# Performance work log

Hardware: AMD Instinct MI355X
Metric: run time of the kernel (lower is better)

Reference implementation:

```python
import jax, jax.numpy as jnp
import numpy as np

# Static config matching init_kwargs
WZ, WH, WW = 2, 6, 12          # window size
MZ, MH, MW = 4, 16, 15          # ceil(input_shape / window_size) for (8,96,180)
HEADS, DIM, B = 6, 192, 1
DH = DIM // HEADS
P = WZ * WH * WW                # 144 tokens per window
WN = MZ * MH * MW               # 960 windows
WT = MZ * MH                    # 64 window types
SCALE = DH ** -0.5
TABLE = WZ * WZ * WH * WH * (2 * WW - 1)  # 3312 bias entries


def _position_index():
    zi = np.arange(WZ); zj = -np.arange(WZ) * WZ
    hi = np.arange(WH); hj = -np.arange(WH) * WH
    w = np.arange(WW)
    c1 = np.stack(np.meshgrid(zi, hi, w, indexing='ij')).reshape(3, -1)  # (3, P)
    c2 = np.stack(np.meshgrid(zj, hj, w, indexing='ij')).reshape(3, -1)  # (3, P)
    coords = (c1[:, :, None] - c2[:, None, :]).transpose(1, 2, 0)        # (P, P, 3)
    coords[:, :, 2] += WW - 1
    coords[:, :, 1] *= 2 * WW - 1
    coords[:, :, 0] *= (2 * WW - 1) * WH * WH
    return coords.sum(-1).reshape(-1)  # (P*P,)

POS_IDX = jnp.asarray(_position_index())


def setup_inputs() -> dict:
    key = jax.random.key(0)
    ks = jax.random.split(key, 5)
    x = jax.random.normal(ks[0], (B * WN, P, DIM), dtype=jnp.float32)
    mask = jnp.zeros((WN, P, P), dtype=jnp.float32)
    w_qkv = jax.random.normal(ks[1], (DIM, 3 * DIM), dtype=jnp.float32) * 0.02
    w_proj = jax.random.normal(ks[2], (DIM, DIM), dtype=jnp.float32) * 0.02
    b_proj = jnp.zeros((DIM,), dtype=jnp.float32)
    bias_table = jax.random.normal(ks[3], (TABLE, WT, HEADS), dtype=jnp.float32) * 0.02
    return {"x": x, "mask": mask, "w_qkv": w_qkv, "w_proj": w_proj,
            "b_proj": b_proj, "bias_table": bias_table}


def reference(x, mask, w_qkv, w_proj, b_proj, bias_table):
    BN = x.shape[0]  # B*WN
    qkv = (x @ w_qkv).reshape(BN, P, 3, HEADS, DH).transpose(2, 0, 3, 1, 4)  # (3,BN,h,P,dh)
    q, k, v = SCALE * qkv[0], qkv[1], qkv[2]
    attn = jnp.einsum('bhid,bhjd->bhij', q, k)  # (BN, h, P, P)
    # (B mZ mH mW) h P P -> (B mW) (mZ mH) h P P
    attn = attn.reshape(B, MZ, MH, MW, HEADS, P, P)
    attn = attn.transpose(0, 3, 1, 2, 4, 5, 6).reshape(B * MW, WT, HEADS, P, P)
    # gather earth-specific bias: (P*P, WT, h) -> (WT, h, P, P)
    bias = bias_table[POS_IDX].reshape(P, P, WT, HEADS).transpose(2, 3, 0, 1)
    attn = attn + bias  # broadcast over (B mW)
    # back to (B mZ mH mW) h P P
    attn = attn.reshape(B, MW, MZ, MH, HEADS, P, P)
    attn = attn.transpose(0, 2, 3, 1, 4, 5, 6).reshape(B, WN, HEADS, P, P)
    attn = attn + mask[None, :, None]  # (1, wN, 1, P, P)
    attn = jax.nn.softmax(attn, axis=-1).reshape(B * WN, HEADS, P, P)
    out = jnp.einsum('bhij,bhjd->bhid', attn, v)           # (BN, h, P, dh)
    out = out.transpose(0, 2, 1, 3).reshape(BN, P, DIM)    # merge heads
    return out @ w_proj + b_proj
```

## Files before the change

### kernel.cpp

```cpp
#include <hip/hip_runtime.h>

#define HEADS 6
#define DIM 192
#define DH 32
#define PW 144
#define WN 960
#define MWD 15
#define NTOK (WN*PW)
#define SCALE 0.17677669529663687f

typedef __attribute__((ext_vector_type(8))) short bf16x8;
typedef __attribute__((ext_vector_type(4))) short bf16x4;
typedef __attribute__((ext_vector_type(4))) float f32x4;

#define MFMA16(a,b,c) __builtin_amdgcn_mfma_f32_16x16x32_bf16(a,b,c,0,0,0)

__device__ __forceinline__ unsigned short f2bf(float f) {
    unsigned int u = __builtin_bit_cast(unsigned int, f);
    u += 0x7fffu + ((u >> 16) & 1u);
    return (unsigned short)(u >> 16);
}
__device__ __forceinline__ float bf2f(unsigned short s) {
    unsigned int u = ((unsigned int)s) << 16;
    return __builtin_bit_cast(float, u);
}

__global__ void prep_weights(const float* __restrict__ wqkv,
                             const float* __restrict__ wproj,
                             unsigned short* __restrict__ wqkvT,
                             unsigned short* __restrict__ wprojT) {
    int t = blockIdx.x * 256 + threadIdx.x;
    if (t < 576 * 192) {
        int n = t / 192, k = t % 192;
        wqkvT[t] = f2bf(wqkv[k * 576 + n]);
    } else {
        int t2 = t - 576 * 192;
        int n = t2 / 192, k = t2 % 192;
        wprojT[t2] = f2bf(wproj[k * 192 + n]);
    }
}

__global__ void prep_bias(const float* __restrict__ table,
                          unsigned short* __restrict__ bias_d) {
    int t = blockIdx.x * 256 + threadIdx.x;
    int j = t % 144;
    int i = (t / 144) % 144;
    int h = (t / 20736) % 6;
    int wt = t / 124416;
    int z1 = i / 72, h1 = (i / 12) % 6, w1 = i % 12;
    int z2 = j / 72, h2 = (j / 12) % 6, w2 = j % 12;
    int pos = (z1 + 2 * z2) * 828 + (h1 + 6 * h2) * 23 + (w1 - w2 + 11);
    bias_d[t] = f2bf(table[pos * 384 + wt * 6 + h]);
}

__global__ __launch_bounds__(256) void prep_cast(const float* __restrict__ x,
                                                 unsigned short* __restrict__ xb) {
    long long c = (long long)blockIdx.x * 256 + threadIdx.x;
    const float* p = x + c * 8;
    f32x4 v0 = *(const f32x4*)p;
    f32x4 v1 = *(const f32x4*)(p + 4);
    bf16x8 o;
    o[0] = (short)f2bf(v0[0]); o[1] = (short)f2bf(v0[1]);
    o[2] = (short)f2bf(v0[2]); o[3] = (short)f2bf(v0[3]);
    o[4] = (short)f2bf(v1[0]); o[5] = (short)f2bf(v1[1]);
    o[6] = (short)f2bf(v1[2]); o[7] = (short)f2bf(v1[3]);
    *(bf16x8*)(xb + c * 8) = o;
}

__global__ __launch_bounds__(256) void qkv_gemm(
        const unsigned short* __restrict__ xb, const unsigned short* __restrict__ wqkvT,
        unsigned short* __restrict__ qb, unsigned short* __restrict__ kb,
        unsigned short* __restrict__ vtb) {
    __shared__ unsigned short A[64 * 200];
    __shared__ unsigned short Bt[96 * 200];
    int bid = blockIdx.x;
    int r8 = bid & 7, s = bid >> 3;
    int nblk = s % 6;
    int mtile = r8 * 270 + s / 6;
    int tid = threadIdx.x;

    const unsigned short* xp = xb + (long long)mtile * (64 * 192);
    #pragma unroll
    for (int it = 0; it < 6; ++it) {
        int c = tid + it * 256;
        int row = c / 24, c8 = (c % 24) * 8;
        *(bf16x8*)&A[row * 200 + c8] = *(const bf16x8*)(xp + c * 8);
    }
    const unsigned short* wp = wqkvT + nblk * (96 * 192);
    #pragma unroll
    for (int it = 0; it < 9; ++it) {
        int c = tid + it * 256;
        int row = c / 24, c8 = (c % 24) * 8;
        *(bf16x8*)&Bt[row * 200 + c8] = *(const bf16x8*)(wp + c * 8);
    }
    __syncthreads();

    int lane = tid & 63, wv = tid >> 6;
    int l16 = lane & 15, quad = lane >> 4;
    f32x4 acc[6];
    #pragma unroll
    for (int i = 0; i < 6; ++i) acc[i] = (f32x4){0.f, 0.f, 0.f, 0.f};

    #pragma unroll
    for (int kc = 0; kc < 6; ++kc) {
        bf16x8 af = *(const bf16x8*)&A[(wv * 16 + l16) * 200 + kc * 32 + quad * 8];
        #pragma unroll
        for (int ct = 0; ct < 6; ++ct) {
            bf16x8 bfr = *(const bf16x8*)&Bt[(ct * 16 + l16) * 200 + kc * 32 + quad * 8];
            acc[ct] = MFMA16(af, bfr, acc[ct]);
        }
    }

    int token0 = mtile * 64 + wv * 16 + quad * 4;
    int win = token0 / 144;
    int p0 = token0 - win * 144;
    #pragma unroll
    for (int ct = 0; ct < 6; ++ct) {
        int c0 = nblk * 96 + ct * 16;
        int which = c0 / 192;
        int head = (c0 % 192) / 32;
        int d = (c0 % 32) + l16;
        if (which == 0) {
            int base = ((win * 6 + head) * 144 + p0) * 32 + d;
            #pragma unroll
            for (int r = 0; r < 4; ++r) qb[base + r * 32] = f2bf(acc[ct][r]);
        } else if (which == 1) {
            int base = ((win * 6 + head) * 144 + p0) * 32 + d;
            #pragma unroll
            for (int r = 0; r < 4; ++r) kb[base + r * 32] = f2bf(acc[ct][r]);
        } else {
            int base = ((win * 6 + head) * 32 + d) * 144 + p0;
            bf16x4 o;
            #pragma unroll
            for (int r = 0; r < 4; ++r) o[r] = (short)f2bf(acc[ct][r]);
            *(bf16x4*)&vtb[base] = o;
        }
    }
}

__global__ __launch_bounds__(192) void attn(
        const unsigned short* __restrict__ qb, const unsigned short* __restrict__ kb,
        const unsigned short* __restrict__ vtb, const unsigned short* __restrict__ bias_d,
        const float* __restrict__ mask, unsigned short* __restrict__ Ob) {
    __shared__ unsigned short Q[144 * 40];
    __shared__ unsigned short Kl[144 * 40];
    __shared__ unsigned short Vt[32 * 160];
    __shared__ unsigned short Pl[3 * 16 * 168];

    int bx = blockIdx.x;
    int r8 = bx & 7, s = bx >> 3;
    int h = s % 6;
    int win = r8 * 120 + s / 6;
    int wt = win / MWD;
    int tid = threadIdx.x;
    int lane = tid & 63, wv = tid >> 6;
    int l16 = lane & 15, quad = lane >> 4;

    int qoff = (win * 6 + h) * (144 * 32);
    #pragma unroll
    for (int it = 0; it < 3; ++it) {
        int c = tid + it * 192;
        int row = c >> 2, c8 = (c & 3) * 8;
        *(bf16x8*)&Q[row * 40 + c8]  = *(const bf16x8*)(qb + qoff + c * 8);
        *(bf16x8*)&Kl[row * 40 + c8] = *(const bf16x8*)(kb + qoff + c * 8);
        int vr = c / 18, vc = (c % 18) * 8;
        *(bf16x8*)&Vt[vr * 160 + vc] = *(const bf16x8*)(vtb + qoff + c * 8);
    }
    {
        int row = lane >> 2, ch = lane & 3;
        *(bf16x4*)&Pl[wv * 2688 + row * 168 + 144 + ch * 4] = (bf16x4){0, 0, 0, 0};
    }
    if (tid < 64) {
        int row = tid >> 1, off = 144 + (tid & 1) * 8;
        *(bf16x8*)&Vt[row * 160 + off] = (bf16x8){0, 0, 0, 0, 0, 0, 0, 0};
    }
    __syncthreads();

    const float* maskp = mask + win * 20736;
    const unsigned short* biasp = bias_d + (wt * 6 + h) * 20736;
    const f32x4 z = {0.f, 0.f, 0.f, 0.f};

    for (int rt = 0; rt < 3; ++rt) {
        int i0 = (wv * 3 + rt) * 16;
        bf16x8 aq = *(const bf16x8*)&Q[(i0 + l16) * 40 + quad * 8];
        f32x4 sreg[9];
        #pragma unroll
        for (int ct = 0; ct < 9; ++ct) {
            bf16x8 bk = *(const bf16x8*)&Kl[(ct * 16 + l16) * 40 + quad * 8];
            sreg[ct] = MFMA16(aq, bk, z);
        }
        #pragma unroll
        for (int ct = 0; ct < 9; ++ct) {
            int j = ct * 16 + l16;
            #pragma unroll
            for (int r = 0; r < 4; ++r) {
                int i = i0 + quad * 4 + r;
                float b = bf2f(biasp[i * 144 + j]);
                float mk = maskp[i * 144 + j];
                sreg[ct][r] = sreg[ct][r] * SCALE + b + mk;
            }
        }
        #pragma unroll
        for (int r = 0; r < 4; ++r) {
            float mx = sreg[0][r];
            #pragma unroll
            for (int ct = 1; ct < 9; ++ct) mx = fmaxf(mx, sreg[ct][r]);
            #pragma unroll
            for (int off = 1; off < 16; off <<= 1) mx = fmaxf(mx, __shfl_xor(mx, off, 64));
            float sum = 0.f;
            #pragma unroll
            for (int ct = 0; ct < 9; ++ct) { float e = __expf(sreg[ct][r] - mx); sreg[ct][r] = e; sum += e; }
            #pragma unroll
            for (int off = 1; off < 16; off <<= 1) sum += __shfl_xor(sum, off, 64);
            float inv = 1.0f / sum;
            #pragma unroll
            for (int ct = 0; ct < 9; ++ct) sreg[ct][r] *= inv;
        }
        int pb = wv * 2688;
        #pragma unroll
        for (int ct = 0; ct < 9; ++ct) {
            #pragma unroll
            for (int r = 0; r < 4; ++r)
                Pl[pb + (quad * 4 + r) * 168 + ct * 16 + l16] = f2bf(sreg[ct][r]);
        }
        f32x4 o0 = z, o1 = z;
        #pragma unroll
        for (int kc = 0; kc < 5; ++kc) {
            bf16x8 ap = *(const bf16x8*)&Pl[pb + l16 * 168 + kc * 32 + quad * 8];
            bf16x8 b0 = *(const bf16x8*)&Vt[l16 * 160 + kc * 32 + quad * 8];
            bf16x8 b1 = *(const bf16x8*)&Vt[(16 + l16) * 160 + kc * 32 + quad * 8];
            o0 = MFMA16(ap, b0, o0);
            o1 = MFMA16(ap, b1, o1);
        }
        #pragma unroll
        for (int r = 0; r < 4; ++r) {
            int i = i0 + quad * 4 + r;
            int ob = (win * 144 + i) * 192 + h * 32 + l16;
            Ob[ob] = f2bf(o0[r]);
            Ob[ob + 16] = f2bf(o1[r]);
        }
    }
}

__global__ __launch_bounds__(256) void out_gemm(
        const unsigned short* __restrict__ Ob, const unsigned short* __restrict__ wprojT,
        const float* __restrict__ bproj, float* __restrict__ out) {
    __shared__ unsigned short A[64 * 200];
    __shared__ unsigned short Bt[96 * 200];
    int bid = blockIdx.x;
    int r8 = bid & 7, s = bid >> 3;
    int nblk = s % 2;
    int mtile = r8 * 270 + s / 2;
    int tid = threadIdx.x;

    const unsigned short* op = Ob + (long long)mtile * (64 * 192);
    #pragma unroll
    for (int it = 0; it < 6; ++it) {
        int c = tid + it * 256;
        int row = c / 24, c8 = (c % 24) * 8;
        *(bf16x8*)&A[row * 200 + c8] = *(const bf16x8*)(op + c * 8);
    }
    const unsigned short* wp = wprojT + nblk * (96 * 192);
    #pragma unroll
    for (int it = 0; it < 9; ++it) {
        int c = tid + it * 256;
        int row = c / 24, c8 = (c % 24) * 8;
        *(bf16x8*)&Bt[row * 200 + c8] = *(const bf16x8*)(wp + c * 8);
    }
    __syncthreads();

    int lane = tid & 63, wv = tid >> 6;
    int l16 = lane & 15, quad = lane >> 4;
    f32x4 acc[6];
    #pragma unroll
    for (int i = 0; i < 6; ++i) acc[i] = (f32x4){0.f, 0.f, 0.f, 0.f};
    #pragma unroll
    for (int kc = 0; kc < 6; ++kc) {
        bf16x8 af = *(const bf16x8*)&A[(wv * 16 + l16) * 200 + kc * 32 + quad * 8];
        #pragma unroll
        for (int ct = 0; ct < 6; ++ct) {
            bf16x8 bfr = *(const bf16x8*)&Bt[(ct * 16 + l16) * 200 + kc * 32 + quad * 8];
            acc[ct] = MFMA16(af, bfr, acc[ct]);
        }
    }
    int token0 = mtile * 64 + wv * 16 + quad * 4;
    #pragma unroll
    for (int ct = 0; ct < 6; ++ct) {
        int c = nblk * 96 + ct * 16 + l16;
        float bp = bproj[c];
        #pragma unroll
        for (int r = 0; r < 4; ++r)
            out[(token0 + r) * 192 + c] = acc[ct][r] + bp;
    }
}

extern "C" void kernel_launch(void* const* d_in, const int* in_sizes, int n_in,
                              void* d_out, int out_size, void* d_ws, size_t ws_size,
                              hipStream_t stream) {
    const float* x     = (const float*)d_in[0];
    const float* mask  = (const float*)d_in[1];
    const float* wqkv  = (const float*)d_in[2];
    const float* wproj = (const float*)d_in[3];
    const float* bproj = (const float*)d_in[4];
    const float* btab  = (const float*)d_in[5];
    float* out = (float*)d_out;

    char* ws = (char*)d_ws;
    unsigned short* xb     = (unsigned short*)(ws + 0);
    unsigned short* Ob     = (unsigned short*)(ws + 0);
    unsigned short* qb     = (unsigned short*)(ws + 53084160);
    unsigned short* kb     = (unsigned short*)(ws + 106168320);
    unsigned short* vtb    = (unsigned short*)(ws + 159252480);
    unsigned short* bias_d = (unsigned short*)(ws + 212336640);
    unsigned short* wqkvT  = (unsigned short*)(ws + 228261888);
    unsigned short* wprojT = (unsigned short*)(ws + 228483072);

    prep_weights<<<576, 256, 0, stream>>>(wqkv, wproj, wqkvT, wprojT);
    prep_bias<<<31104, 256, 0, stream>>>(btab, bias_d);
    prep_cast<<<12960, 256, 0, stream>>>(x, xb);
    qkv_gemm<<<12960, 256, 0, stream>>>(xb, wqkvT, qb, kb, vtb);
    attn<<<5760, 192, 0, stream>>>(qb, kb, vtb, bias_d, mask, Ob);
    out_gemm<<<4320, 256, 0, stream>>>(Ob, wprojT, bproj, out);
}
```

Measured before the change: 486.0 us.

## Pre-permute bias and mask into MFMA fragment layout and fuse x cast into QKV GEMM

Bias and mask are rearranged by prep kernels into per-lane contiguous bf16 fragments matching the MFMA accumulator layout, so attn loads them with a few 16-byte vector loads instead of scattered scalar loads. The mask is converted to bf16, halving its traffic in attn, at the cost of an extra full pass over the fp32 mask each call and reduced mask precision. The separate fp32-to-bf16 cast kernel for x is folded into the QKV GEMM tile load, removing an intermediate buffer round trip. Q is read directly from global memory rather than staged in LDS, and attn gets an occupancy hint.

```diff
diff --git a/kernel.cpp b/kernel.cpp
--- a/kernel.cpp
+++ b/kernel.cpp
@@ -6,7 +6,6 @@
 #define PW 144
 #define WN 960
 #define MWD 15
-#define NTOK (WN*PW)
 #define SCALE 0.17677669529663687f
 
 typedef __attribute__((ext_vector_type(8))) short bf16x8;
@@ -40,35 +39,53 @@
     }
 }
 
-__global__ void prep_bias(const float* __restrict__ table,
-                          unsigned short* __restrict__ bias_d) {
+__global__ __launch_bounds__(256) void prep_biasR(const float* __restrict__ table,
+                                                  unsigned short* __restrict__ biasR) {
     int t = blockIdx.x * 256 + threadIdx.x;
-    int j = t % 144;
-    int i = (t / 144) % 144;
-    int h = (t / 20736) % 6;
-    int wt = t / 124416;
-    int z1 = i / 72, h1 = (i / 12) % 6, w1 = i % 12;
-    int z2 = j / 72, h2 = (j / 12) % 6, w2 = j % 12;
-    int pos = (z1 + 2 * z2) * 828 + (h1 + 6 * h2) * 23 + (w1 - w2 + 11);
-    bias_d[t] = f2bf(table[pos * 384 + wt * 6 + h]);
-}
-
-__global__ __launch_bounds__(256) void prep_cast(const float* __restrict__ x,
-                                                 unsigned short* __restrict__ xb) {
-    long long c = (long long)blockIdx.x * 256 + threadIdx.x;
-    const float* p = x + c * 8;
-    f32x4 v0 = *(const f32x4*)p;
-    f32x4 v1 = *(const f32x4*)(p + 4);
-    bf16x8 o;
-    o[0] = (short)f2bf(v0[0]); o[1] = (short)f2bf(v0[1]);
-    o[2] = (short)f2bf(v0[2]); o[3] = (short)f2bf(v0[3]);
-    o[4] = (short)f2bf(v1[0]); o[5] = (short)f2bf(v1[1]);
-    o[6] = (short)f2bf(v1[2]); o[7] = (short)f2bf(v1[3]);
-    *(bf16x8*)(xb + c * 8) = o;
+    int e = t % 40;
+    int u = t / 40;
+    int lane = u & 63;
+    int u2 = u >> 6;
+    int it = u2 % 9;
+    int u3 = u2 / 9;
+    int h = u3 % 6;
+    int wt = u3 / 6;
+    unsigned short v = 0;
+    if (e < 36) {
+        int ct = e >> 2, r = e & 3;
+        int quad = lane >> 4, l16 = lane & 15;
+        int i = it * 16 + quad * 4 + r;
+        int j = ct * 16 + l16;
+        int z1 = i / 72, h1 = (i / 12) % 6, w1 = i % 12;
+        int z2 = j / 72, h2 = (j / 12) % 6, w2 = j % 12;
+        int pos = (z1 + 2 * z2) * 828 + (h1 + 6 * h2) * 23 + (w1 - w2 + 11);
+        v = f2bf(table[pos * 384 + wt * 6 + h]);
+    }
+    biasR[t] = v;
+}
+
+__global__ __launch_bounds__(256) void prep_maskR(const float* __restrict__ mask,
+                                                  unsigned short* __restrict__ maskR) {
+    int t = blockIdx.x * 256 + threadIdx.x;
+    int e = t % 40;
+    int u = t / 40;
+    int lane = u & 63;
+    int u2 = u >> 6;
+    int it = u2 % 9;
+    int win = u2 / 9;
+    unsigned short v = 0;
+    if (e < 36) {
+        int ct = e >> 2, r = e & 3;
+        int quad = lane >> 4, l16 = lane & 15;
+        int i = it * 16 + quad * 4 + r;
+        int j = ct * 16 + l16;
+        v = f2bf(mask[win * 20736 + i * 144 + j]);
+    }
+    maskR[t] = v;
 }
 
 __global__ __launch_bounds__(256) void qkv_gemm(
-        const unsigned short* __restrict__ xb, const unsigned short* __restrict__ wqkvT,
+        const float* __restrict__ x, const unsigned short* __restrict__ wqkvT,
         unsigned short* __restrict__ qb, unsigned short* __restrict__ kb,
         unsigned short* __restrict__ vtb) {
     __shared__ unsigned short A[64 * 200];
@@ -79,12 +96,16 @@
     int mtile = r8 * 270 + s / 6;
     int tid = threadIdx.x;
 
-    const unsigned short* xp = xb + (long long)mtile * (64 * 192);
-    #pragma unroll
-    for (int it = 0; it < 6; ++it) {
+    const float* xp = x + (long long)mtile * (64 * 192);
+    #pragma unroll
+    for (int it = 0; it < 12; ++it) {
         int c = tid + it * 256;
-        int row = c / 24, c8 = (c % 24) * 8;
-        *(bf16x8*)&A[row * 200 + c8] = *(const bf16x8*)(xp + c * 8);
+        int row = c / 48, c4 = c % 48;
+        f32x4 v = *(const f32x4*)(xp + row * 192 + c4 * 4);
+        bf16x4 o;
+        o[0] = (short)f2bf(v[0]); o[1] = (short)f2bf(v[1]);
+        o[2] = (short)f2bf(v[2]); o[3] = (short)f2bf(v[3]);
+        *(bf16x4*)&A[row * 200 + c4 * 4] = o;
     }
     const unsigned short* wp = wqkvT + nblk * (96 * 192);
     #pragma unroll
@@ -138,11 +159,10 @@
     }
 }
 
-__global__ __launch_bounds__(192) void attn(
+__global__ __launch_bounds__(192, 4) void attn(
         const unsigned short* __restrict__ qb, const unsigned short* __restrict__ kb,
-        const unsigned short* __restrict__ vtb, const unsigned short* __restrict__ bias_d,
-        const float* __restrict__ mask, unsigned short* __restrict__ Ob) {
-    __shared__ unsigned short Q[144 * 40];
+        const unsigned short* __restrict__ vtb, const unsigned short* __restrict__ biasR,
+        const unsigned short* __restrict__ maskR, unsigned short* __restrict__ Ob) {
     __shared__ unsigned short Kl[144 * 40];
     __shared__ unsigned short Vt[32 * 160];
     __shared__ unsigned short Pl[3 * 16 * 168];
@@ -161,7 +181,6 @@
     for (int it = 0; it < 3; ++it) {
         int c = tid + it * 192;
         int row = c >> 2, c8 = (c & 3) * 8;
-        *(bf16x8*)&Q[row * 40 + c8]  = *(const bf16x8*)(qb + qoff + c * 8);
         *(bf16x8*)&Kl[row * 40 + c8] = *(const bf16x8*)(kb + qoff + c * 8);
         int vr = c / 18, vc = (c % 18) * 8;
         *(bf16x8*)&Vt[vr * 160 + vc] = *(const bf16x8*)(vtb + qoff + c * 8);
@@ -176,13 +195,20 @@
     }
     __syncthreads();
 
-    const float* maskp = mask + win * 20736;
-    const unsigned short* biasp = bias_d + (wt * 6 + h) * 20736;
+    const unsigned short* bR = biasR + ((wt * 6 + h) * 9) * 2560 + lane * 40;
+    const unsigned short* mR = maskR + (win * 9) * 2560 + lane * 40;
     const f32x4 z = {0.f, 0.f, 0.f, 0.f};
 
     for (int rt = 0; rt < 3; ++rt) {
-        int i0 = (wv * 3 + rt) * 16;
-        bf16x8 aq = *(const bf16x8*)&Q[(i0 + l16) * 40 + quad * 8];
+        int it = wv * 3 + rt;
+        int i0 = it * 16;
+        bf16x8 aq = *(const bf16x8*)(qb + qoff + (i0 + l16) * 32 + quad * 8);
+        bf16x8 bb[5], mm[5];
+        #pragma unroll
+        for (int w = 0; w < 5; ++w) {
+            bb[w] = *(const bf16x8*)(bR + it * 2560 + w * 8);
+            mm[w] = *(const bf16x8*)(mR + it * 2560 + w * 8);
+        }
         f32x4 sreg[9];
         #pragma unroll
         for (int ct = 0; ct < 9; ++ct) {
@@ -191,13 +217,12 @@
         }
         #pragma unroll
         for (int ct = 0; ct < 9; ++ct) {
-            int j = ct * 16 + l16;
             #pragma unroll
             for (int r = 0; r < 4; ++r) {
-                int i = i0 + quad * 4 + r;
-                float b = bf2f(biasp[i * 144 + j]);
-                float mk = maskp[i * 144 + j];
-                sreg[ct][r] = sreg[ct][r] * SCALE + b + mk;
+                int e = ct * 4 + r;
+                sreg[ct][r] = sreg[ct][r] * SCALE
+                            + bf2f((unsigned short)bb[e >> 3][e & 7])
+                            + bf2f((unsigned short)mm[e >> 3][e & 7]);
             }
         }
         #pragma unroll
@@ -306,19 +331,19 @@
     float* out = (float*)d_out;
 
     char* ws = (char*)d_ws;
-    unsigned short* xb     = (unsigned short*)(ws + 0);
     unsigned short* Ob     = (unsigned short*)(ws + 0);
     unsigned short* qb     = (unsigned short*)(ws + 53084160);
     unsigned short* kb     = (unsigned short*)(ws + 106168320);
     unsigned short* vtb    = (unsigned short*)(ws + 159252480);
-    unsigned short* bias_d = (unsigned short*)(ws + 212336640);
-    unsigned short* wqkvT  = (unsigned short*)(ws + 228261888);
-    unsigned short* wprojT = (unsigned short*)(ws + 228483072);
+    unsigned short* biasR  = (unsigned short*)(ws + 212336640);
+    unsigned short* maskR  = (unsigned short*)(ws + 230031360);
+    unsigned short* wqkvT  = (unsigned short*)(ws + 274268160);
+    unsigned short* wprojT = (unsigned short*)(ws + 274489344);
 
     prep_weights<<<576, 256, 0, stream>>>(wqkv, wproj, wqkvT, wprojT);
-    prep_bias<<<31104, 256, 0, stream>>>(btab, bias_d);
-    prep_cast<<<12960, 256, 0, stream>>>(x, xb);
-    qkv_gemm<<<12960, 256, 0, stream>>>(xb, wqkvT, qb, kb, vtb);
-    attn<<<5760, 192, 0, stream>>>(qb, kb, vtb, bias_d, mask, Ob);
+    prep_biasR<<<34560, 256, 0, stream>>>(btab, biasR);
+    prep_maskR<<<86400, 256, 0, stream>>>(mask, maskR);
+    qkv_gemm<<<12960, 256, 0, stream>>>(x, wqkvT, qb, kb, vtb);
+    attn<<<5760, 192, 0, stream>>>(qb, kb, vtb, biasR, maskR, Ob);
     out_gemm<<<4320, 256, 0, stream>>>(Ob, wprojT, bproj, out);
 }
```

Result: slower. 561.2 us (+15.5%).
